# Optimization experiments

Hardware: AMD Instinct MI355X
Metric: run time of the kernel (lower is better)

Reference implementation:

```python
import jax, jax.numpy as jnp
import numpy as np

def setup_inputs() -> dict:
    key = jax.random.key(0)
    k1, k2, k3, k4, k5 = jax.random.split(key, 5)
    vocab, embed, hidden = 32000, 1024, 1024
    batch, src_len = 64, 512
    src = jax.random.randint(k1, (batch, src_len), 0, vocab)
    emb_table = jax.random.normal(k2, (vocab, embed), dtype=jnp.float32)
    # xavier_uniform bounds
    bx = float(np.sqrt(6.0 / (embed + hidden)))
    bh = float(np.sqrt(6.0 / (hidden + hidden)))
    W_xh = jax.random.uniform(k3, (hidden, embed), minval=-bx, maxval=bx, dtype=jnp.float32)
    b_xh = jax.random.uniform(k4, (hidden,), minval=-1.0/np.sqrt(embed), maxval=1.0/np.sqrt(embed), dtype=jnp.float32)
    W_hh = jax.random.uniform(k5, (hidden, hidden), minval=-bh, maxval=bh, dtype=jnp.float32)
    return {"src": src, "emb_table": emb_table, "W_xh": W_xh, "b_xh": b_xh, "W_hh": W_hh}

def reference(src, emb_table, W_xh, b_xh, W_hh):
    # embedded: (batch, src_len, embed)
    embedded = emb_table[src]
    # precompute input projection for all timesteps: (batch, src_len, hidden)
    x_proj = jnp.einsum('bte,he->bth', embedded, W_xh) + b_xh
    batch = src.shape[0]
    hidden = W_hh.shape[0]
    h0 = jnp.zeros((batch, hidden), dtype=jnp.float32)

    def step(h, x_t):
        h_new = jnp.tanh(x_t + h @ W_hh.T)
        return h_new, None

    # scan over time: x_proj transposed to (src_len, batch, hidden)
    h_final, _ = jax.lax.scan(step, h0, jnp.swapaxes(x_proj, 0, 1))
    return h_final
```

## Files before the change

kernel.cpp:

```cpp
#include <hip/hip_runtime.h>
#include <hip/hip_fp16.h>

typedef _Float16 half8 __attribute__((ext_vector_type(8)));
typedef float floatx4 __attribute__((ext_vector_type(4)));

#define HBUF_BYTES (2ull * 16 * 1024 * 8)
#define CTL_BYTES  (32ull * 1024)
#define XP_OFF     (HBUF_BYTES + CTL_BYTES)
#define XP_BYTES   (512ull * 64 * 1024 * 2)
#define FLAG_STRIDE 16

union pack4 { unsigned long long u; _Float16 h[4]; };

__device__ inline half8 cvt8(const float4 a, const float4 b) {
    half8 r;
    r[0] = (_Float16)a.x; r[1] = (_Float16)a.y; r[2] = (_Float16)a.z; r[3] = (_Float16)a.w;
    r[4] = (_Float16)b.x; r[5] = (_Float16)b.y; r[6] = (_Float16)b.z; r[7] = (_Float16)b.w;
    return r;
}

__global__ __launch_bounds__(256) void xproj_kernel(
    const int* __restrict__ src, const float* __restrict__ emb,
    const float* __restrict__ Wxh, const float* __restrict__ bxh,
    _Float16* __restrict__ xp)
{
    __shared__ _Float16 As[128][40];
    __shared__ _Float16 Bs[128][40];

    const int tid  = threadIdx.x;
    const int lane = tid & 63;
    const int w    = tid >> 6;
    const int m15  = lane & 15;
    const int quad = lane >> 4;
    const int bid  = blockIdx.x;
    const int bn   = bid & 7;
    const int bm   = bid >> 3;
    const int m0   = bm * 128, n0 = bn * 128;
    const int wm   = w & 1, wn = w >> 1;

    const int  srow = tid >> 1;
    const int  scol = (tid & 1) * 16;
    const long arow = (long)src[m0 + srow] * 1024;
    const float* abase = emb + arow + scol;
    const float* bbase = Wxh + (long)(n0 + srow) * 1024 + scol;

    floatx4 zero4 = {0.f, 0.f, 0.f, 0.f};
    floatx4 acc[4][4];
#pragma unroll
    for (int mt = 0; mt < 4; mt++)
#pragma unroll
        for (int nt = 0; nt < 4; nt++) acc[mt][nt] = zero4;

    for (int k0 = 0; k0 < 1024; k0 += 32) {
        __syncthreads();
        float4 a0 = *(const float4*)(abase + k0);
        float4 a1 = *(const float4*)(abase + k0 + 4);
        float4 a2 = *(const float4*)(abase + k0 + 8);
        float4 a3 = *(const float4*)(abase + k0 + 12);
        float4 b0 = *(const float4*)(bbase + k0);
        float4 b1 = *(const float4*)(bbase + k0 + 4);
        float4 b2 = *(const float4*)(bbase + k0 + 8);
        float4 b3 = *(const float4*)(bbase + k0 + 12);
        *(half8*)&As[srow][scol]     = cvt8(a0, a1);
        *(half8*)&As[srow][scol + 8] = cvt8(a2, a3);
        *(half8*)&Bs[srow][scol]     = cvt8(b0, b1);
        *(half8*)&Bs[srow][scol + 8] = cvt8(b2, b3);
        __syncthreads();

        half8 af[4], bf[4];
#pragma unroll
        for (int mt = 0; mt < 4; mt++)
            af[mt] = *(const half8*)&As[wm * 64 + mt * 16 + m15][quad * 8];
#pragma unroll
        for (int nt = 0; nt < 4; nt++)
            bf[nt] = *(const half8*)&Bs[wn * 64 + nt * 16 + m15][quad * 8];
#pragma unroll
        for (int mt = 0; mt < 4; mt++)
#pragma unroll
            for (int nt = 0; nt < 4; nt++)
                acc[mt][nt] = __builtin_amdgcn_mfma_f32_16x16x32_f16(
                    af[mt], bf[nt], acc[mt][nt], 0, 0, 0);
    }

#pragma unroll
    for (int nt = 0; nt < 4; nt++) {
        const int n = n0 + wn * 64 + nt * 16 + m15;
        const float bias = bxh[n];
#pragma unroll
        for (int mt = 0; mt < 4; mt++) {
            const int mrow = m0 + wm * 64 + mt * 16 + quad * 4;
#pragma unroll
            for (int r = 0; r < 4; r++) {
                const int m = mrow + r;
                const int b = m >> 9;
                const int t = m & 511;
                xp[((long)t * 64 + b) * 1024 + n] = (_Float16)(acc[mt][nt][r] + bias);
            }
        }
    }
}

__global__ __launch_bounds__(256, 1) void rnn_kernel(
    const float* __restrict__ Whh, const _Float16* __restrict__ xp,
    unsigned long long* __restrict__ hb, int* __restrict__ flags,
    float* __restrict__ out)
{
    __shared__ _Float16 hstage[16][1032];
    __shared__ floatx4  cred[4][4][64];

    const int tid    = threadIdx.x;
    const int lane   = tid & 63;
    const int w      = tid >> 6;
    const int m15    = lane & 15;
    const int quad   = lane >> 4;
    const int wg     = blockIdx.x;
    const int g      = wg & 15;
    const int member = wg >> 4;
    const int b0     = g * 4;

    for (int i = tid; i < 16 * 1032; i += 256) ((_Float16*)hstage)[i] = (_Float16)0.f;

    half8 Wf[4][8];
#pragma unroll
    for (int nt = 0; nt < 4; nt++) {
        const float* wrow = Whh + (long)(member * 64 + nt * 16 + m15) * 1024
                                + w * 256 + quad * 8;
#pragma unroll
        for (int kk = 0; kk < 8; kk++) {
            float4 lo = *(const float4*)(wrow + kk * 32);
            float4 hi = *(const float4*)(wrow + kk * 32 + 4);
            Wf[nt][kk] = cvt8(lo, hi);
        }
    }
    __syncthreads();

    const int dim = member * 64 + w * 16 + m15;
    float xv[4] = {0.f, 0.f, 0.f, 0.f};
    if (quad == 0) {
#pragma unroll
        for (int r = 0; r < 4; r++)
            xv[r] = (float)xp[((long)0 * 64 + b0 + r) * 1024 + dim];
    }

    int* myflag = flags + (g * 16 + member) * FLAG_STRIDE;
    const int* gflags = flags + g * 16 * FLAG_STRIDE;
    floatx4 zero4 = {0.f, 0.f, 0.f, 0.f};

    for (int t = 0; t < 512; t++) {
        const unsigned long long* hcu = hb + (size_t)(t & 1) * 16384 + (size_t)g * 1024;
        unsigned long long*       hnu = hb + (size_t)((t + 1) & 1) * 16384 + (size_t)g * 1024;

        if (t > 0) {
            if (tid < 16) {
                const int* fw = gflags + tid * FLAG_STRIDE;
                while (__hip_atomic_load(fw, __ATOMIC_RELAXED,
                                         __HIP_MEMORY_SCOPE_AGENT) < t) { }
            }
            __syncthreads();
        }

        {
            unsigned long long v[4];
#pragma unroll
            for (int i = 0; i < 4; i++)
                v[i] = __hip_atomic_load(hcu + tid + 256 * i, __ATOMIC_RELAXED,
                                         __HIP_MEMORY_SCOPE_AGENT);
#pragma unroll
            for (int i = 0; i < 4; i++) {
                pack4 p; p.u = v[i];
                const int d = tid + 256 * i;
#pragma unroll
                for (int b = 0; b < 4; b++) hstage[b][d] = p.h[b];
            }
        }
        __syncthreads();

        floatx4 pacc[4];
#pragma unroll
        for (int nt = 0; nt < 4; nt++) pacc[nt] = zero4;
#pragma unroll
        for (int kk = 0; kk < 8; kk++) {
            half8 a = *(const half8*)&hstage[m15][w * 256 + kk * 32 + quad * 8];
#pragma unroll
            for (int nt = 0; nt < 4; nt++)
                pacc[nt] = __builtin_amdgcn_mfma_f32_16x16x32_f16(
                    a, Wf[nt][kk], pacc[nt], 0, 0, 0);
        }

#pragma unroll
        for (int nt = 0; nt < 4; nt++) cred[w][nt][lane] = pacc[nt];
        __syncthreads();
        floatx4 dsum = cred[0][w][lane];
#pragma unroll
        for (int ww = 1; ww < 4; ww++) dsum += cred[ww][w][lane];

        if (quad == 0) {
            pack4 p;
#pragma unroll
            for (int r = 0; r < 4; r++) {
                float pre  = dsum[r] + xv[r];
                float e    = __expf(2.0f * pre);
                float hval = 1.0f - 2.0f / (e + 1.0f);
                p.h[r] = (_Float16)hval;
                if (t == 511) out[(b0 + r) * 1024 + dim] = hval;
            }
            __hip_atomic_store(hnu + dim, p.u, __ATOMIC_RELAXED,
                               __HIP_MEMORY_SCOPE_AGENT);
        }

        __syncthreads();
        if (tid == 0)
            __hip_atomic_store(myflag, t + 1, __ATOMIC_RELAXED,
                               __HIP_MEMORY_SCOPE_AGENT);

        if (t < 511 && quad == 0) {
#pragma unroll
            for (int r = 0; r < 4; r++)
                xv[r] = (float)xp[((long)(t + 1) * 64 + b0 + r) * 1024 + dim];
        }
    }
}

extern "C" void kernel_launch(void* const* d_in, const int* in_sizes, int n_in,
                              void* d_out, int out_size, void* d_ws, size_t ws_size,
                              hipStream_t stream) {
    const int*   src = (const int*)d_in[0];
    const float* emb = (const float*)d_in[1];
    const float* Wxh = (const float*)d_in[2];
    const float* bxh = (const float*)d_in[3];
    const float* Whh = (const float*)d_in[4];
    float* out = (float*)d_out;

    char* ws = (char*)d_ws;
    unsigned long long* hb = (unsigned long long*)ws;
    int* flags = (int*)(ws + HBUF_BYTES);
    _Float16* xp = (_Float16*)(ws + XP_OFF);

    hipMemsetAsync(ws, 0, HBUF_BYTES + CTL_BYTES, stream);

    hipLaunchKernelGGL(xproj_kernel, dim3(2048), dim3(256), 0, stream,
                       src, emb, Wxh, bxh, xp);

    hipLaunchKernelGGL(rnn_kernel, dim3(256), dim3(256), 0, stream,
                       Whh, xp, hb, flags, out);
}
```

Measured before the change: 1.313 ms.

## Replace per-step flag barrier with tagged hidden-state words polled directly

Drops the separate per-workgroup flag array and spin-wait barrier. Each hidden-state 64-bit word now carries a 16-bit timestep tag next to two fp16 values, so consumers poll the data words until every tag matches the current step. This removes one flag round trip and a trailing __syncthreads per timestep on the sequential recurrence path. In exchange the hidden buffer doubles in size and readers do more loads plus bit unpacking.

```diff
diff --git a/kernel.cpp b/kernel.cpp
--- a/kernel.cpp
+++ b/kernel.cpp
@@ -4,13 +4,11 @@
 typedef _Float16 half8 __attribute__((ext_vector_type(8)));
 typedef float floatx4 __attribute__((ext_vector_type(4)));
 
-#define HBUF_BYTES (2ull * 16 * 1024 * 8)
-#define CTL_BYTES  (32ull * 1024)
-#define XP_OFF     (HBUF_BYTES + CTL_BYTES)
+#define HBUF_BYTES (2ull * 16 * 1024 * 2 * 8)
+#define XP_OFF     HBUF_BYTES
 #define XP_BYTES   (512ull * 64 * 1024 * 2)
-#define FLAG_STRIDE 16
-
-union pack4 { unsigned long long u; _Float16 h[4]; };
+
+union hbits { _Float16 f; unsigned short s; };
 
 __device__ inline half8 cvt8(const float4 a, const float4 b) {
     half8 r;
@@ -102,8 +100,7 @@
 
 __global__ __launch_bounds__(256, 1) void rnn_kernel(
     const float* __restrict__ Whh, const _Float16* __restrict__ xp,
-    unsigned long long* __restrict__ hb, int* __restrict__ flags,
-    float* __restrict__ out)
+    unsigned long long* __restrict__ hb, float* __restrict__ out)
 {
     __shared__ _Float16 hstage[16][1032];
     __shared__ floatx4  cred[4][4][64];
@@ -142,35 +139,40 @@
             xv[r] = (float)xp[((long)0 * 64 + b0 + r) * 1024 + dim];
     }
 
-    int* myflag = flags + (g * 16 + member) * FLAG_STRIDE;
-    const int* gflags = flags + g * 16 * FLAG_STRIDE;
     floatx4 zero4 = {0.f, 0.f, 0.f, 0.f};
 
     for (int t = 0; t < 512; t++) {
-        const unsigned long long* hcu = hb + (size_t)(t & 1) * 16384 + (size_t)g * 1024;
-        unsigned long long*       hnu = hb + (size_t)((t + 1) & 1) * 16384 + (size_t)g * 1024;
-
-        if (t > 0) {
-            if (tid < 16) {
-                const int* fw = gflags + tid * FLAG_STRIDE;
-                while (__hip_atomic_load(fw, __ATOMIC_RELAXED,
-                                         __HIP_MEMORY_SCOPE_AGENT) < t) { }
-            }
-            __syncthreads();
-        }
-
         {
-            unsigned long long v[4];
-#pragma unroll
-            for (int i = 0; i < 4; i++)
-                v[i] = __hip_atomic_load(hcu + tid + 256 * i, __ATOMIC_RELAXED,
+            const unsigned long long* hg =
+                hb + (size_t)(t & 1) * 32768 + (size_t)g * 2048 + (size_t)tid * 8;
+            const unsigned tagu = (unsigned)t;
+            unsigned long long v[8];
+#pragma unroll
+            for (int j = 0; j < 8; j++)
+                v[j] = __hip_atomic_load(hg + j, __ATOMIC_RELAXED,
                                          __HIP_MEMORY_SCOPE_AGENT);
-#pragma unroll
-            for (int i = 0; i < 4; i++) {
-                pack4 p; p.u = v[i];
-                const int d = tid + 256 * i;
-#pragma unroll
-                for (int b = 0; b < 4; b++) hstage[b][d] = p.h[b];
+            for (;;) {
+                unsigned bad = 0;
+#pragma unroll
+                for (int j = 0; j < 8; j++)
+                    if ((unsigned)(v[j] & 0xffffu) != tagu) bad |= (1u << j);
+                if (!bad) break;
+#pragma unroll
+                for (int j = 0; j < 8; j++)
+                    if (bad & (1u << j))
+                        v[j] = __hip_atomic_load(hg + j, __ATOMIC_RELAXED,
+                                                 __HIP_MEMORY_SCOPE_AGENT);
+            }
+#pragma unroll
+            for (int b = 0; b < 4; b++) {
+                unsigned long long q = 0;
+#pragma unroll
+                for (int e = 0; e < 4; e++) {
+                    unsigned long long x =
+                        (v[e * 2 + (b >> 1)] >> (16 + 16 * (b & 1))) & 0xffffu;
+                    q |= x << (16 * e);
+                }
+                *(unsigned long long*)&hstage[b][tid * 4] = q;
             }
         }
         __syncthreads();
@@ -195,23 +197,26 @@
         for (int ww = 1; ww < 4; ww++) dsum += cred[ww][w][lane];
 
         if (quad == 0) {
-            pack4 p;
+            hbits hv[4];
 #pragma unroll
             for (int r = 0; r < 4; r++) {
                 float pre  = dsum[r] + xv[r];
                 float e    = __expf(2.0f * pre);
                 float hval = 1.0f - 2.0f / (e + 1.0f);
-                p.h[r] = (_Float16)hval;
+                hv[r].f = (_Float16)hval;
                 if (t == 511) out[(b0 + r) * 1024 + dim] = hval;
             }
-            __hip_atomic_store(hnu + dim, p.u, __ATOMIC_RELAXED,
-                               __HIP_MEMORY_SCOPE_AGENT);
-        }
-
-        __syncthreads();
-        if (tid == 0)
-            __hip_atomic_store(myflag, t + 1, __ATOMIC_RELAXED,
-                               __HIP_MEMORY_SCOPE_AGENT);
+            const unsigned long long tag1 = (unsigned long long)(unsigned)(t + 1);
+            unsigned long long w0 = tag1 | ((unsigned long long)hv[0].s << 16)
+                                         | ((unsigned long long)hv[1].s << 32);
+            unsigned long long w1 = tag1 | ((unsigned long long)hv[2].s << 16)
+                                         | ((unsigned long long)hv[3].s << 32);
+            unsigned long long* hw =
+                hb + (size_t)((t + 1) & 1) * 32768 + (size_t)g * 2048
+                   + (size_t)dim * 2;
+            __hip_atomic_store(hw,     w0, __ATOMIC_RELAXED, __HIP_MEMORY_SCOPE_AGENT);
+            __hip_atomic_store(hw + 1, w1, __ATOMIC_RELAXED, __HIP_MEMORY_SCOPE_AGENT);
+        }
 
         if (t < 511 && quad == 0) {
 #pragma unroll
@@ -233,14 +238,13 @@
 
     char* ws = (char*)d_ws;
     unsigned long long* hb = (unsigned long long*)ws;
-    int* flags = (int*)(ws + HBUF_BYTES);
     _Float16* xp = (_Float16*)(ws + XP_OFF);
 
-    hipMemsetAsync(ws, 0, HBUF_BYTES + CTL_BYTES, stream);
+    hipMemsetAsync(ws, 0, HBUF_BYTES, stream);
 
     hipLaunchKernelGGL(xproj_kernel, dim3(2048), dim3(256), 0, stream,
                        src, emb, Wxh, bxh, xp);
 
     hipLaunchKernelGGL(rnn_kernel, dim3(256), dim3(256), 0, stream,
-                       Whh, xp, hb, flags, out);
-}
+                       Whh, xp, hb, out);
+}
```

Result: slower. 1.648 ms (+25.4%).
